# Kernel optimization log

Hardware: AMD Instinct MI355X
Metric: run time of the kernel (lower is better)

## Reference

```python
import jax, jax.numpy as jnp
import numpy as np

B, N, DIM, H, K = 2, 8192, 256, 8, 32
HD = DIM // H


def setup_inputs() -> dict:
    key = jax.random.key(0)
    ks = jax.random.split(key, 10)
    s = 1.0 / np.sqrt(DIM)
    return {
        "x": jax.random.normal(ks[0], (B, N, DIM), jnp.float32),
        "xyz": jax.random.normal(ks[1], (B, N, 3), jnp.float32),
        "idx": jax.random.randint(ks[2], (B, N, K), 0, N, jnp.int32),
        "Wq": jax.random.normal(ks[3], (DIM, DIM), jnp.float32) * s,
        "bq": jnp.zeros((DIM,), jnp.float32),
        "Wk": jax.random.normal(ks[4], (DIM, DIM), jnp.float32) * s,
        "bk": jnp.zeros((DIM,), jnp.float32),
        "Wv": jax.random.normal(ks[5], (DIM, DIM), jnp.float32) * s,
        "bv": jnp.zeros((DIM,), jnp.float32),
        "Wo": jax.random.normal(ks[6], (DIM, DIM), jnp.float32) * s,
        "bo": jnp.zeros((DIM,), jnp.float32),
        "W1": jax.random.normal(ks[7], (3, 32), jnp.float32) * 0.5,
        "b1": jnp.zeros((32,), jnp.float32),
        "W2": jax.random.normal(ks[8], (32, H), jnp.float32) * 0.2,
        "b2": jnp.zeros((H,), jnp.float32),
    }


def reference(x, xyz, idx, Wq, bq, Wk, bk, Wv, bv, Wo, bo, W1, b1, W2, b2):
    Bn, Nn, C = x.shape
    k = idx.shape[-1]
    q = (x @ Wq + bq).reshape(Bn, Nn, H, HD)          # [B,N,H,hd]
    kf = (x @ Wk + bk).reshape(Bn, Nn, H, HD)
    vf = (x @ Wv + bv).reshape(Bn, Nn, H, HD)
    # gather k neighbors per point (per-batch fancy indexing)
    gather = jax.vmap(lambda f, i: f[i])               # [N,H,hd],[N,k] -> [N,k,H,hd]
    kn = gather(kf, idx)                               # [B,N,k,H,hd]
    vn = gather(vf, idx)
    nxyz = jax.vmap(lambda p, i: p[i])(xyz, idx)       # [B,N,k,3]
    rel = xyz[:, :, None, :] - nxyz                    # [B,N,k,3]
    bias = jax.nn.relu(rel @ W1 + b1) @ W2 + b2        # [B,N,k,H]
    scores = jnp.einsum('bnhd,bnkhd->bnhk', q, kn) / np.sqrt(HD).astype(np.float32)
    scores = scores + bias.transpose(0, 1, 3, 2)       # [B,N,H,k]
    attn = jax.nn.softmax(scores, axis=-1)
    out = jnp.einsum('bnhk,bnkhd->bnhd', attn, vn).reshape(Bn, Nn, C)
    return out @ Wo + bo
```

## Files before the change

### kernel.cpp

```cpp
#include <hip/hip_runtime.h>
#include <hip/hip_bf16.h>

typedef unsigned int uint32;
typedef unsigned short ushort;
typedef __attribute__((ext_vector_type(4))) float floatx4;
typedef __attribute__((ext_vector_type(8))) __bf16 bf16x8;

#define NPTS 8192
#define HSZ 524288
#define HSZ2 1048576

__device__ __forceinline__ ushort f2bf(float f) {
    uint32 u = __float_as_uint(f);
    uint32 r = (u + 0x7fffu + ((u >> 16) & 1u)) >> 16;
    return (ushort)r;
}
__device__ __forceinline__ float bf1(ushort u) { return __uint_as_float((uint32)u << 16); }
__device__ __forceinline__ float bflo(uint32 u) { return __uint_as_float(u << 16); }
__device__ __forceinline__ float bfhi(uint32 u) { return __uint_as_float(u & 0xffff0000u); }

__global__ __launch_bounds__(256) void prep_kernel(
    const float* __restrict__ x, const float* __restrict__ xyz, const int* __restrict__ idx,
    const float* __restrict__ Wq, const float* __restrict__ Wk,
    const float* __restrict__ Wv, const float* __restrict__ Wo,
    const float* __restrict__ bq, const float* __restrict__ bk, const float* __restrict__ bv,
    const float* __restrict__ W1, const float* __restrict__ b1,
    const float* __restrict__ W2, const float* __restrict__ b2,
    ushort* __restrict__ xb, ushort* __restrict__ Wqkvt, ushort* __restrict__ Wot,
    float* __restrict__ biasqkv, ushort* __restrict__ bias_hg) {
    const int bi = blockIdx.x;
    const int tid = threadIdx.x;
    if (bi < 4096) {
        int i = (bi * 256 + tid) * 4;
        float4 v = *(const float4*)(x + i);
        ushort4 o;
        o.x = f2bf(v.x); o.y = f2bf(v.y); o.z = f2bf(v.z); o.w = f2bf(v.w);
        *(ushort4*)(xb + i) = o;
    } else if (bi < 5120) {
        int f = (bi - 4096) * 256 + tid;
        if (f < 768 * 256) {
            int n = f >> 8, k = f & 255;
            int seg = n >> 8, nc = n & 255;
            const float* W = (seg == 0) ? Wq : (seg == 1) ? Wk : Wv;
            Wqkvt[f] = f2bf(W[k * 256 + nc]);
        } else {
            int g = f - 768 * 256;
            int n = g >> 8, k = g & 255;
            Wot[g] = f2bf(Wo[k * 256 + n]);
        }
        if (f < 768) biasqkv[f] = (f < 256) ? bq[f] : (f < 512) ? bk[f - 256] : bv[f - 512];
    } else {
        __shared__ float W1s[96], b1s[32], W2s[256], b2s[8];
        if (tid < 96) W1s[tid] = W1[tid];
        if (tid < 32) b1s[tid] = b1[tid];
        W2s[tid] = W2[tid];
        if (tid < 8) b2s[tid] = b2[tid];
        __syncthreads();
        const int wid = tid >> 6, lane = tid & 63;
        const int s = lane >> 5, j = lane & 31;
        const int p = (bi - 5120) * 8 + wid * 2 + s;
        const int b = p >> 13, n = p & 8191;
        const int nj = idx[(size_t)p * 32 + j];
        const size_t pb = ((size_t)b * NPTS + n) * 3;
        const size_t nb = ((size_t)b * NPTS + nj) * 3;
        const float rx = xyz[pb + 0] - xyz[nb + 0];
        const float ry = xyz[pb + 1] - xyz[nb + 1];
        const float rz = xyz[pb + 2] - xyz[nb + 2];
        float acc[8];
#pragma unroll
        for (int h = 0; h < 8; ++h) acc[h] = b2s[h];
#pragma unroll
        for (int u = 0; u < 32; ++u) {
            float hv = rx * W1s[u] + ry * W1s[32 + u] + rz * W1s[64 + u] + b1s[u];
            hv = fmaxf(hv, 0.f);
#pragma unroll
            for (int h = 0; h < 8; ++h) acc[h] += hv * W2s[u * 8 + h];
        }
#pragma unroll
        for (int h = 0; h < 8; ++h) bias_hg[(size_t)h * HSZ + p * 32 + j] = f2bf(acc[h]);
    }
}

__global__ __launch_bounds__(256) void gemm_qkv(const ushort* __restrict__ A,
                                                const ushort* __restrict__ Wt,
                                                const float* __restrict__ bias,
                                                ushort* __restrict__ qh,
                                                ushort* __restrict__ kvh) {
    __shared__ __align__(16) ushort As[128 * 64];
    __shared__ __align__(16) ushort Bs[128 * 64];
    const int tid = threadIdx.x;
    const int w = tid >> 6, lane = tid & 63;
    const int m0 = blockIdx.y * 128, n0 = blockIdx.x * 128;
    const int wm = (w & 1) * 64, wn = (w >> 1) * 64;

    floatx4 acc[4][4] = {};

    for (int kt = 0; kt < 256; kt += 64) {
        __syncthreads();
#pragma unroll
        for (int c4 = 0; c4 < 4; ++c4) {
            const int c = w * 4 + c4;
            const int r = c * 8 + (lane >> 3);
            const int gseg = (lane & 7) ^ (r & 7);
            const char* ga = (const char*)(A + (size_t)(m0 + r) * 256 + kt) + gseg * 16;
            const char* gb = (const char*)(Wt + (size_t)(n0 + r) * 256 + kt) + gseg * 16;
            __builtin_amdgcn_global_load_lds((const __attribute__((address_space(1))) void*)ga,
                                             (__attribute__((address_space(3))) void*)((char*)As + c * 1024),
                                             16, 0, 0);
            __builtin_amdgcn_global_load_lds((const __attribute__((address_space(1))) void*)gb,
                                             (__attribute__((address_space(3))) void*)((char*)Bs + c * 1024),
                                             16, 0, 0);
        }
        __syncthreads();

        bf16x8 af[2][4], bg[2][4];
#pragma unroll
        for (int kk = 0; kk < 2; ++kk) {
            const int s = kk * 4 + (lane >> 4);
            const int phys = s ^ (lane & 7);
#pragma unroll
            for (int i = 0; i < 4; ++i) {
                af[kk][i] = *(const bf16x8*)((const char*)As + (wm + i * 16 + (lane & 15)) * 128 + phys * 16);
                bg[kk][i] = *(const bf16x8*)((const char*)Bs + (wn + i * 16 + (lane & 15)) * 128 + phys * 16);
            }
        }
#pragma unroll
        for (int kk = 0; kk < 2; ++kk)
#pragma unroll
            for (int mi = 0; mi < 4; ++mi)
#pragma unroll
                for (int ni = 0; ni < 4; ++ni)
                    acc[mi][ni] = __builtin_amdgcn_mfma_f32_16x16x32_bf16(af[kk][mi], bg[kk][ni], acc[mi][ni], 0, 0, 0);
    }

#pragma unroll
    for (int ni = 0; ni < 4; ++ni) {
        const int col = n0 + wn + ni * 16 + (lane & 15);
        const int seg = col >> 8;
        const int head = (col >> 5) & 7;
        const int dim = (col & 31) + ((seg == 2) ? 32 : 0);
        const float bv = bias[col];
#pragma unroll
        for (int mi = 0; mi < 4; ++mi) {
            const int row0 = m0 + wm + mi * 16 + (lane >> 4) * 4;
#pragma unroll
            for (int r = 0; r < 4; ++r) {
                const int row = row0 + r;
                const ushort val = f2bf(acc[mi][ni][r] + bv);
                if (seg == 0)
                    qh[(size_t)head * HSZ + (size_t)row * 32 + dim] = val;
                else
                    kvh[(size_t)head * HSZ2 + (size_t)row * 64 + dim] = val;
            }
        }
    }
}

__global__ __launch_bounds__(256) void gemm_mfma64(const ushort* __restrict__ A,
                                                   const ushort* __restrict__ Wt,
                                                   const float* __restrict__ bias,
                                                   float* __restrict__ outv, int N) {
    __shared__ __align__(16) ushort As[64 * 32];
    __shared__ __align__(16) ushort Bs[64 * 32];
    const int tid = threadIdx.x;
    const int w = tid >> 6, lane = tid & 63;
    const int m0 = blockIdx.y * 64, n0 = blockIdx.x * 64;
    const int row = tid >> 2;
    const int col16 = (tid & 3) * 16;

    floatx4 acc[4] = {};

    for (int kt = 0; kt < 256; kt += 32) {
        __syncthreads();
        {
            const char* ga = (const char*)(A + (size_t)(m0 + row) * 256 + kt) + col16;
            const char* gb = (const char*)(Wt + (size_t)(n0 + row) * 256 + kt) + col16;
            __builtin_amdgcn_global_load_lds((const __attribute__((address_space(1))) void*)ga,
                                             (__attribute__((address_space(3))) void*)((char*)As + w * 1024),
                                             16, 0, 0);
            __builtin_amdgcn_global_load_lds((const __attribute__((address_space(1))) void*)gb,
                                             (__attribute__((address_space(3))) void*)((char*)Bs + w * 1024),
                                             16, 0, 0);
        }
        __syncthreads();

        bf16x8 af = *(const bf16x8*)&As[(w * 16 + (lane & 15)) * 32 + (lane >> 4) * 8];
        bf16x8 bg[4];
#pragma unroll
        for (int ni = 0; ni < 4; ++ni)
            bg[ni] = *(const bf16x8*)&Bs[(ni * 16 + (lane & 15)) * 32 + (lane >> 4) * 8];
#pragma unroll
        for (int ni = 0; ni < 4; ++ni)
            acc[ni] = __builtin_amdgcn_mfma_f32_16x16x32_bf16(af, bg[ni], acc[ni], 0, 0, 0);
    }

#pragma unroll
    for (int ni = 0; ni < 4; ++ni) {
        const int col = n0 + ni * 16 + (lane & 15);
        const float bv = bias[col];
        const int row0 = m0 + w * 16 + (lane >> 4) * 4;
#pragma unroll
        for (int r = 0; r < 4; ++r)
            outv[(size_t)(row0 + r) * N + col] = acc[ni][r] + bv;
    }
}

__global__ __launch_bounds__(256) void attn_kernel(
    const ushort* __restrict__ qh, const ushort* __restrict__ kvh,
    const int* __restrict__ idx, const ushort* __restrict__ bias_hg, ushort* __restrict__ out) {
    const int tid = threadIdx.x, wid = tid >> 6, lane = tid & 63;
    const int h = blockIdx.x >> 10;
    const int pg = blockIdx.x & 1023;
    const int pbase = pg * 16 + wid * 4;

    const char* kv_h = (const char*)(kvh + (size_t)h * HSZ2);

    const int s = lane >> 4;
    const int g = (lane >> 2) & 3, q4 = lane & 3;
    const int p = pbase + s;
    const int b = p >> 13;

    const int4 n0 = *(const int4*)(idx + (size_t)p * 32 + g * 8);
    const int4 n1 = *(const int4*)(idx + (size_t)p * 32 + g * 8 + 4);
    const uint4 qp = *(const uint4*)(qh + (size_t)h * HSZ + p * 32 + q4 * 8);
    const uint4 bs = *(const uint4*)(bias_hg + (size_t)h * HSZ + p * 32 + g * 8);

    const uint32 roff = (uint32)(b * NPTS);
    uint32 addr[8];
    addr[0] = ((uint32)n0.x + roff) * 128u + q4 * 16;
    addr[1] = ((uint32)n0.y + roff) * 128u + q4 * 16;
    addr[2] = ((uint32)n0.z + roff) * 128u + q4 * 16;
    addr[3] = ((uint32)n0.w + roff) * 128u + q4 * 16;
    addr[4] = ((uint32)n1.x + roff) * 128u + q4 * 16;
    addr[5] = ((uint32)n1.y + roff) * 128u + q4 * 16;
    addr[6] = ((uint32)n1.z + roff) * 128u + q4 * 16;
    addr[7] = ((uint32)n1.w + roff) * 128u + q4 * 16;

    uint4 kreg[8], vreg[8];
#pragma unroll
    for (int i = 0; i < 8; ++i) kreg[i] = *(const uint4*)(kv_h + addr[i]);
#pragma unroll
    for (int i = 0; i < 8; ++i) vreg[i] = *(const uint4*)(kv_h + addr[i] + 64);

    const float4 qa = {bflo(qp.x), bfhi(qp.x), bflo(qp.y), bfhi(qp.y)};
    const float4 qb = {bflo(qp.z), bfhi(qp.z), bflo(qp.w), bfhi(qp.w)};

    float e_r[8];
    float esum = 0.f;
#pragma unroll
    for (int i = 0; i < 8; ++i) {
        const uint4 kv = kreg[i];
        float d = bflo(kv.x) * qa.x + bfhi(kv.x) * qa.y
                + bflo(kv.y) * qa.z + bfhi(kv.y) * qa.w
                + bflo(kv.z) * qb.x + bfhi(kv.z) * qb.y
                + bflo(kv.w) * qb.z + bfhi(kv.w) * qb.w;
        d += __shfl_xor(d, 1, 64);
        d += __shfl_xor(d, 2, 64);
        const uint32 bw = (i < 2) ? bs.x : (i < 4) ? bs.y : (i < 6) ? bs.z : bs.w;
        const float bb = (i & 1) ? bfhi(bw) : bflo(bw);
        const float e = __expf(d * 0.17677669529663687f + bb);
        e_r[i] = e;
        esum += e;
    }
    float ssum = esum;
    ssum += __shfl_xor(ssum, 4, 64);
    ssum += __shfl_xor(ssum, 8, 64);
    const float rinv = __builtin_amdgcn_rcpf(ssum);

    float a0 = 0.f, a1 = 0.f, a2 = 0.f, a3 = 0.f, a4 = 0.f, a5 = 0.f, a6 = 0.f, a7 = 0.f;
#pragma unroll
    for (int i = 0; i < 8; ++i) {
        const float wgt = e_r[i];
        const uint4 v = vreg[i];
        a0 += wgt * bflo(v.x); a1 += wgt * bfhi(v.x);
        a2 += wgt * bflo(v.y); a3 += wgt * bfhi(v.y);
        a4 += wgt * bflo(v.z); a5 += wgt * bfhi(v.z);
        a6 += wgt * bflo(v.w); a7 += wgt * bfhi(v.w);
    }
    const bool hi4 = (lane & 4) != 0;
    {
        float t0 = hi4 ? a0 : a4, t1 = hi4 ? a1 : a5, t2 = hi4 ? a2 : a6, t3 = hi4 ? a3 : a7;
        float k0 = hi4 ? a4 : a0, k1 = hi4 ? a5 : a1, k2 = hi4 ? a6 : a2, k3 = hi4 ? a7 : a3;
        a0 = k0 + __shfl_xor(t0, 4, 64);
        a1 = k1 + __shfl_xor(t1, 4, 64);
        a2 = k2 + __shfl_xor(t2, 4, 64);
        a3 = k3 + __shfl_xor(t3, 4, 64);
    }
    const bool hi8 = (lane & 8) != 0;
    {
        float t0 = hi8 ? a0 : a2, t1 = hi8 ? a1 : a3;
        float k0 = hi8 ? a2 : a0, k1 = hi8 ? a3 : a1;
        a0 = k0 + __shfl_xor(t0, 8, 64);
        a1 = k1 + __shfl_xor(t1, 8, 64);
    }
    const int D = q4 * 8 + (hi4 ? 4 : 0) + (hi8 ? 2 : 0);
    const uint32 u = (uint32)f2bf(a0 * rinv) | ((uint32)f2bf(a1 * rinv) << 16);
    *(uint32*)(out + (size_t)p * 256 + h * 32 + D) = u;
}

extern "C" void kernel_launch(void* const* d_in, const int* in_sizes, int n_in,
                              void* d_out, int out_size, void* d_ws, size_t ws_size,
                              hipStream_t stream) {
    const float* x   = (const float*)d_in[0];
    const float* xyz = (const float*)d_in[1];
    const int*   idx = (const int*)d_in[2];
    const float* Wq = (const float*)d_in[3];
    const float* bq = (const float*)d_in[4];
    const float* Wk = (const float*)d_in[5];
    const float* bk = (const float*)d_in[6];
    const float* Wv = (const float*)d_in[7];
    const float* bv = (const float*)d_in[8];
    const float* Wo = (const float*)d_in[9];
    const float* bo = (const float*)d_in[10];
    const float* W1 = (const float*)d_in[11];
    const float* b1 = (const float*)d_in[12];
    const float* W2 = (const float*)d_in[13];
    const float* b2 = (const float*)d_in[14];

    char* wsb = (char*)d_ws;
    ushort* x_bf    = (ushort*)wsb;
    ushort* aout_bf = x_bf;
    ushort* qh      = (ushort*)(wsb + 8388608);
    ushort* kvh     = (ushort*)(wsb + 16777216);
    ushort* bias_hg = (ushort*)(wsb + 33554432);
    ushort* Wqkvt   = (ushort*)(wsb + 41943040);
    ushort* Wot     = (ushort*)(wsb + 42336256);
    float*  biasqkv = (float*)(wsb + 42467328);

    prep_kernel<<<7168, 256, 0, stream>>>(x, xyz, idx, Wq, Wk, Wv, Wo, bq, bk, bv,
                                          W1, b1, W2, b2, x_bf, Wqkvt, Wot, biasqkv, bias_hg);

    gemm_qkv<<<dim3(6, 128), 256, 0, stream>>>(x_bf, Wqkvt, biasqkv, qh, kvh);

    attn_kernel<<<8192, 256, 0, stream>>>(qh, kvh, idx, bias_hg, aout_bf);

    gemm_mfma64<<<dim3(4, 256), 256, 0, stream>>>(aout_bf, Wot, bo, (float*)d_out, 256);
}
```

Measured before the change: 174.0 us.

## Enlarge output-projection GEMM tiles to 128x128 with XOR-swizzled LDS

The output projection GEMM moves from 64x64 tiles with a K step of 32 to 128x128 tiles with a K step of 64. Each wave now computes a 64x64 sub-tile, which raises MFMA reuse per LDS load. The LDS layout uses an XOR swizzle to avoid bank conflicts. The launch drops from 1024 blocks to 256, which lowers occupancy and parallelism for a small GEMM (M=16384, N=K=256).

```diff
diff --git a/kernel.cpp b/kernel.cpp
--- a/kernel.cpp
+++ b/kernel.cpp
@@ -156,52 +156,68 @@
     }
 }
 
-__global__ __launch_bounds__(256) void gemm_mfma64(const ushort* __restrict__ A,
-                                                   const ushort* __restrict__ Wt,
-                                                   const float* __restrict__ bias,
-                                                   float* __restrict__ outv, int N) {
-    __shared__ __align__(16) ushort As[64 * 32];
-    __shared__ __align__(16) ushort Bs[64 * 32];
+__global__ __launch_bounds__(256) void gemm_oproj(const ushort* __restrict__ A,
+                                                  const ushort* __restrict__ Wt,
+                                                  const float* __restrict__ bias,
+                                                  float* __restrict__ outv) {
+    __shared__ __align__(16) ushort As[128 * 64];
+    __shared__ __align__(16) ushort Bs[128 * 64];
     const int tid = threadIdx.x;
     const int w = tid >> 6, lane = tid & 63;
-    const int m0 = blockIdx.y * 64, n0 = blockIdx.x * 64;
-    const int row = tid >> 2;
-    const int col16 = (tid & 3) * 16;
-
-    floatx4 acc[4] = {};
-
-    for (int kt = 0; kt < 256; kt += 32) {
-        __syncthreads();
-        {
-            const char* ga = (const char*)(A + (size_t)(m0 + row) * 256 + kt) + col16;
-            const char* gb = (const char*)(Wt + (size_t)(n0 + row) * 256 + kt) + col16;
+    const int m0 = blockIdx.y * 128, n0 = blockIdx.x * 128;
+    const int wm = (w & 1) * 64, wn = (w >> 1) * 64;
+
+    floatx4 acc[4][4] = {};
+
+    for (int kt = 0; kt < 256; kt += 64) {
+        __syncthreads();
+#pragma unroll
+        for (int c4 = 0; c4 < 4; ++c4) {
+            const int c = w * 4 + c4;
+            const int r = c * 8 + (lane >> 3);
+            const int gseg = (lane & 7) ^ (r & 7);
+            const char* ga = (const char*)(A + (size_t)(m0 + r) * 256 + kt) + gseg * 16;
+            const char* gb = (const char*)(Wt + (size_t)(n0 + r) * 256 + kt) + gseg * 16;
             __builtin_amdgcn_global_load_lds((const __attribute__((address_space(1))) void*)ga,
-                                             (__attribute__((address_space(3))) void*)((char*)As + w * 1024),
+                                             (__attribute__((address_space(3))) void*)((char*)As + c * 1024),
                                              16, 0, 0);
             __builtin_amdgcn_global_load_lds((const __attribute__((address_space(1))) void*)gb,
-                                             (__attribute__((address_space(3))) void*)((char*)Bs + w * 1024),
+                                             (__attribute__((address_space(3))) void*)((char*)Bs + c * 1024),
                                              16, 0, 0);
         }
         __syncthreads();
 
-        bf16x8 af = *(const bf16x8*)&As[(w * 16 + (lane & 15)) * 32 + (lane >> 4) * 8];
-        bf16x8 bg[4];
-#pragma unroll
-        for (int ni = 0; ni < 4; ++ni)
-            bg[ni] = *(const bf16x8*)&Bs[(ni * 16 + (lane & 15)) * 32 + (lane >> 4) * 8];
-#pragma unroll
-        for (int ni = 0; ni < 4; ++ni)
-            acc[ni] = __builtin_amdgcn_mfma_f32_16x16x32_bf16(af, bg[ni], acc[ni], 0, 0, 0);
+        bf16x8 af[2][4], bg[2][4];
+#pragma unroll
+        for (int kk = 0; kk < 2; ++kk) {
+            const int s = kk * 4 + (lane >> 4);
+            const int phys = s ^ (lane & 7);
+#pragma unroll
+            for (int i = 0; i < 4; ++i) {
+                af[kk][i] = *(const bf16x8*)((const char*)As + (wm + i * 16 + (lane & 15)) * 128 + phys * 16);
+                bg[kk][i] = *(const bf16x8*)((const char*)Bs + (wn + i * 16 + (lane & 15)) * 128 + phys * 16);
+            }
+        }
+#pragma unroll
+        for (int kk = 0; kk < 2; ++kk)
+#pragma unroll
+            for (int mi = 0; mi < 4; ++mi)
+#pragma unroll
+                for (int ni = 0; ni < 4; ++ni)
+                    acc[mi][ni] = __builtin_amdgcn_mfma_f32_16x16x32_bf16(af[kk][mi], bg[kk][ni], acc[mi][ni], 0, 0, 0);
     }
 
 #pragma unroll
     for (int ni = 0; ni < 4; ++ni) {
-        const int col = n0 + ni * 16 + (lane & 15);
+        const int col = n0 + wn + ni * 16 + (lane & 15);
         const float bv = bias[col];
-        const int row0 = m0 + w * 16 + (lane >> 4) * 4;
-#pragma unroll
-        for (int r = 0; r < 4; ++r)
-            outv[(size_t)(row0 + r) * N + col] = acc[ni][r] + bv;
+#pragma unroll
+        for (int mi = 0; mi < 4; ++mi) {
+            const int row0 = m0 + wm + mi * 16 + (lane >> 4) * 4;
+#pragma unroll
+            for (int r = 0; r < 4; ++r)
+                outv[(size_t)(row0 + r) * 256 + col] = acc[mi][ni][r] + bv;
+        }
     }
 }
 
@@ -334,5 +350,5 @@
 
     attn_kernel<<<8192, 256, 0, stream>>>(qh, kvh, idx, bias_hg, aout_bf);
 
-    gemm_mfma64<<<dim3(4, 256), 256, 0, stream>>>(aout_bf, Wot, bo, (float*)d_out, 256);
-}
+    gemm_oproj<<<dim3(2, 128), 256, 0, stream>>>(aout_bf, Wot, bo, (float*)d_out);
+}
```

Result: no change. 172.4 us (median of 2 runs) (-0.9%).
